# Performance work log

Measured on AMD Instinct MI355X. Metric: run time of the kernel, lower is better.

Reference implementation:

```python
import jax, jax.numpy as jnp
import numpy as np


def _lsa(cost):
    """Exact rectangular linear sum assignment (Jonker-Volgenant / e-maxx
    Hungarian with potentials). Returns (row_ind, col_ind) matching
    scipy.optimize.linear_sum_assignment (row_ind sorted ascending)."""
    n, m = cost.shape
    transposed = n > m
    if transposed:
        cost = cost.T
        n, m = m, n
    cost = np.asarray(cost, dtype=np.float64)
    INF = 1e18
    u = np.zeros(n + 1)
    v = np.zeros(m + 1)
    p = np.zeros(m + 1, dtype=np.int64)   # p[j]: 1-based row assigned to col j
    way = np.zeros(m + 1, dtype=np.int64)
    for i in range(1, n + 1):
        p[0] = i
        j0 = 0
        minv = np.full(m + 1, INF)
        used = np.zeros(m + 1, dtype=bool)
        while True:
            used[j0] = True
            i0 = p[j0]
            cur = cost[i0 - 1] - u[i0] - v[1:]          # vectorized over cols
            upd = (~used[1:]) & (cur < minv[1:])
            minv[1:] = np.where(upd, cur, minv[1:])
            way[1:] = np.where(upd, j0, way[1:])
            masked = np.where(used[1:], INF, minv[1:])
            j1 = int(np.argmin(masked)) + 1
            delta = masked[j1 - 1]
            u[p[used]] += delta
            v[used] -= delta
            minv[1:] = np.where(used[1:], minv[1:], minv[1:] - delta)
            j0 = j1
            if p[j0] == 0:
                break
        while j0 != 0:
            j1 = way[j0]
            p[j0] = p[j1]
            j0 = j1
    if transposed:
        pairs = sorted((j - 1, p[j] - 1) for j in range(1, m + 1) if p[j] != 0)
    else:
        pairs = sorted((p[j] - 1, j - 1) for j in range(1, m + 1) if p[j] != 0)
    row_ind = np.array([r for r, _ in pairs], dtype=np.int64)
    col_ind = np.array([c for _, c in pairs], dtype=np.int64)
    return row_ind, col_ind


def _row_order(cost_b):
    """Matched rows first (scipy order), then unmatched rows sorted ascending."""
    N = cost_b.shape[0]
    row_ind, _ = _lsa(cost_b)
    remain = sorted(set(range(N)) - set(row_ind.tolist()))
    return np.concatenate([row_ind, np.asarray(remain, dtype=np.int64)])


def _pairwise_l2(seq1, seq2):
    # Fused batched cdist: ||a-b|| = sqrt(|a|^2 + |b|^2 - 2 a.b)
    a2 = jnp.sum(seq1 * seq1, axis=-1)[:, :, None]   # [B,N,1]
    b2 = jnp.sum(seq2 * seq2, axis=-1)[:, None, :]   # [B,1,M]
    ab = jnp.einsum('bnd,bmd->bnm', seq1, seq2)      # [B,N,M]
    return jnp.sqrt(jnp.maximum(a2 + b2 - 2.0 * ab, 0.0))


def setup_inputs() -> dict:
    key = jax.random.key(0)
    k1, k2 = jax.random.split(key)
    B, N, M, D = 16, 512, 448, 1536
    return {
        'seq1': jax.random.normal(k1, (B, N, D), dtype=jnp.float32),
        'seq2': jax.random.normal(k2, (B, M, D), dtype=jnp.float32),
    }


def reference(seq1, seq2):
    cost = np.asarray(_pairwise_l2(seq1, seq2))      # [B,N,M], one fused kernel
    # Hungarian solve is inherently sequential / CPU-bound per batch element.
    perm = np.stack([_row_order(cost[b]) for b in range(cost.shape[0])], 0)
    perm = jnp.asarray(perm)                         # [B,N]
    return jnp.take_along_axis(seq1, perm[:, :, None], axis=1)
```

## Files before the change

kernel.cpp:

```cpp
#include <hip/hip_runtime.h>
#include <math.h>

#define BB 16
#define NN 512
#define MM 448
#define DD 1536

constexpr int TK = 32;

__global__ __launch_bounds__(256) void cost_kernel(const float* __restrict__ s1,
                                                   const float* __restrict__ s2,
                                                   float* __restrict__ Ct) {
  __shared__ float As[TK][68];
  __shared__ float Bs[TK][68];
  const int b = blockIdx.z;
  const int ibase = blockIdx.x * 64;
  const int jbase = blockIdx.y * 64;
  const int tid = threadIdx.x;
  const float* s1b = s1 + ((size_t)b * NN + ibase) * DD;
  const float* s2b = s2 + ((size_t)b * MM + jbase) * DD;
  const int ix = (tid & 15) * 4;
  const int jy = (tid >> 4) * 4;
  double acc[16];
#pragma unroll
  for (int t = 0; t < 16; ++t) acc[t] = 0.0;

  for (int k0 = 0; k0 < DD; k0 += TK) {
#pragma unroll
    for (int rep = 0; rep < 2; ++rep) {
      int idx = tid + rep * 256;
      int r = idx >> 3;
      int c4 = (idx & 7) * 4;
      float4 a = *(const float4*)(s1b + (size_t)r * DD + k0 + c4);
      As[c4 + 0][r] = a.x; As[c4 + 1][r] = a.y; As[c4 + 2][r] = a.z; As[c4 + 3][r] = a.w;
      float4 bb = *(const float4*)(s2b + (size_t)r * DD + k0 + c4);
      Bs[c4 + 0][r] = bb.x; Bs[c4 + 1][r] = bb.y; Bs[c4 + 2][r] = bb.z; Bs[c4 + 3][r] = bb.w;
    }
    __syncthreads();
    float pacc[16];
#pragma unroll
    for (int t = 0; t < 16; ++t) pacc[t] = 0.f;
#pragma unroll 8
    for (int kk = 0; kk < TK; ++kk) {
      float4 av = *(const float4*)&As[kk][ix];
      float4 bv = *(const float4*)&Bs[kk][jy];
      float a[4] = {av.x, av.y, av.z, av.w};
      float bq[4] = {bv.x, bv.y, bv.z, bv.w};
#pragma unroll
      for (int t = 0; t < 4; ++t)
#pragma unroll
        for (int q = 0; q < 4; ++q) {
          float d = a[t] - bq[q];
          pacc[t * 4 + q] = fmaf(d, d, pacc[t * 4 + q]);
        }
    }
#pragma unroll
    for (int t = 0; t < 16; ++t) acc[t] += (double)pacc[t];
    __syncthreads();
  }
#pragma unroll
  for (int t = 0; t < 4; ++t)
#pragma unroll
    for (int q = 0; q < 4; ++q) {
      int i = ibase + ix + t;
      int jj = jbase + jy + q;
      float d2 = (float)acc[t * 4 + q];
      Ct[((size_t)b * MM + jj) * NN + i] = sqrtf(fmaxf(d2, 0.f));
    }
}

__device__ __forceinline__ double wave_min_bcast_f64(double x) {
  union DU { double d; unsigned int u[2]; };
  DU v; v.d = x;
  DU inf; inf.d = 1e18;
#define DPP_STEP(CTRL) { DU o; \
  o.u[0] = (unsigned)__builtin_amdgcn_update_dpp((int)inf.u[0], (int)v.u[0], CTRL, 0xF, 0xF, false); \
  o.u[1] = (unsigned)__builtin_amdgcn_update_dpp((int)inf.u[1], (int)v.u[1], CTRL, 0xF, 0xF, false); \
  if (o.d < v.d) v.d = o.d; }
  DPP_STEP(0x111)
  DPP_STEP(0x112)
  DPP_STEP(0x114)
  DPP_STEP(0x118)
  DPP_STEP(0x142)
  DPP_STEP(0x143)
#undef DPP_STEP
  DU r;
  r.u[0] = (unsigned)__builtin_amdgcn_readlane((int)v.u[0], 63);
  r.u[1] = (unsigned)__builtin_amdgcn_readlane((int)v.u[1], 63);
  return r.d;
}

__global__ __launch_bounds__(64) void jv_kernel(const float* __restrict__ Ct,
                                                int* __restrict__ perm) {
  const int b = blockIdx.x;
  const float* C = Ct + (size_t)b * MM * NN;
  __shared__ double u_lds[MM + 1];
  __shared__ int p_lds[NN + 1];
  __shared__ int way_lds[NN + 1];
  __shared__ int cnt_lds[64];
  const int lane = threadIdx.x;
  const int jbase = 8 * lane + 1;

  for (int t = lane; t <= MM; t += 64) u_lds[t] = 0.0;
  for (int t = lane; t <= NN; t += 64) { p_lds[t] = 0; way_lds[t] = 0; }
  double vcol[8];
#pragma unroll
  for (int q = 0; q < 8; ++q) vcol[q] = 0.0;
  asm volatile("s_waitcnt lgkmcnt(0)" ::: "memory");

  for (int i = 1; i <= MM; ++i) {
    if (lane == 0) p_lds[0] = i;
    double minv[8], rec[8];
    int preg[8];
#pragma unroll
    for (int q = 0; q < 8; ++q) { minv[q] = 1e18; rec[q] = 0.0; preg[q] = 0; }
    int usedm = 0;
    double cum = 0.0;
    int j0 = 0, i0 = i;

    while (true) {
#pragma unroll
      for (int q = 0; q < 8; ++q)
        if (j0 == jbase + q) { usedm |= (1 << q); preg[q] = i0; rec[q] = cum; }

      const float4* r4 = (const float4*)(C + (size_t)(i0 - 1) * NN);
      float4 ca = r4[2 * lane];
      float4 cb = r4[2 * lane + 1];
      double uu = u_lds[i0];
      float c[8] = {ca.x, ca.y, ca.z, ca.w, cb.x, cb.y, cb.z, cb.w};
#pragma unroll
      for (int q = 0; q < 8; ++q) {
        if (!((usedm >> q) & 1)) {
          double cur = ((double)c[q] - uu) - vcol[q];
          if (cur < minv[q]) { minv[q] = cur; way_lds[jbase + q] = j0; }
        }
      }
      double cand = 1e18; int argj = 0;
#pragma unroll
      for (int q = 0; q < 8; ++q) {
        double mq = ((usedm >> q) & 1) ? 1e18 : minv[q];
        if (mq < cand) { cand = mq; argj = jbase + q; }
      }
      double delta = wave_min_bcast_f64(cand);
      unsigned long long bm = __ballot(cand == delta);
      int sl = (int)__ffsll((unsigned long long)bm) - 1;
      int j1 = __builtin_amdgcn_readlane(argj, sl);
      cum += delta;
#pragma unroll
      for (int q = 0; q < 8; ++q)
        if (!((usedm >> q) & 1)) minv[q] -= delta;
      int pn = p_lds[j1];
      j0 = j1;
      if (pn == 0) break;
      i0 = pn;
    }

    if (lane == 0) u_lds[i] += cum;
#pragma unroll
    for (int q = 0; q < 8; ++q)
      if ((usedm >> q) & 1) {
        double d = cum - rec[q];
        vcol[q] -= d;
        u_lds[preg[q]] += d;
      }
    asm volatile("s_waitcnt lgkmcnt(0)" ::: "memory");
    if (lane == 0) {
      int jj = j0;
      while (jj != 0) { int jp = way_lds[jj]; p_lds[jj] = p_lds[jp]; jj = jp; }
    }
    asm volatile("s_waitcnt lgkmcnt(0)" ::: "memory");
  }

  int mask = 0, cnt = 0;
#pragma unroll
  for (int q = 0; q < 8; ++q)
    if (p_lds[jbase + q] != 0) { mask |= 1 << q; cnt++; }
  cnt_lds[lane] = cnt;
  asm volatile("s_waitcnt lgkmcnt(0)" ::: "memory");
  int pre = 0;
  for (int l = 0; l < 64; ++l) { int cl = cnt_lds[l]; if (l < lane) pre += cl; }
  int mpos = pre;
  int upos = MM + (8 * lane - pre);
#pragma unroll
  for (int q = 0; q < 8; ++q) {
    int col = 8 * lane + q;
    if ((mask >> q) & 1) perm[b * NN + mpos++] = col;
    else                 perm[b * NN + upos++] = col;
  }
}

__global__ __launch_bounds__(256) void gather_kernel(const float* __restrict__ s1,
                                                     const int* __restrict__ perm,
                                                     float* __restrict__ out) {
  const int bi = blockIdx.x;
  const int b = bi >> 9;
  const int src = perm[bi];
  const float4* sp = (const float4*)(s1 + ((size_t)b * NN + src) * DD);
  float4* dp = (float4*)(out + (size_t)bi * DD);
  for (int t = threadIdx.x; t < DD / 4; t += 256) dp[t] = sp[t];
}

extern "C" void kernel_launch(void* const* d_in, const int* in_sizes, int n_in,
                              void* d_out, int out_size, void* d_ws, size_t ws_size,
                              hipStream_t stream) {
  const float* s1 = (const float*)d_in[0];
  const float* s2 = (const float*)d_in[1];
  float* out = (float*)d_out;
  float* Ct = (float*)d_out;
  int* perm = (int*)d_ws;

  dim3 cg(NN / 64, MM / 64, BB);
  cost_kernel<<<cg, 256, 0, stream>>>(s1, s2, Ct);
  jv_kernel<<<BB, 64, 0, stream>>>(Ct, perm);
  gather_kernel<<<BB * NN, 256, 0, stream>>>(s1, perm, out);
}
```

Measured before the change: 7.982 ms.

## Warm-start Hungarian solver with greedy row-minimum matching and dual potentials

Before the augmenting-path loop, each row's minimum cost and argmin column are computed with a wave reduction. The row potential is set to that minimum, and the row is greedily assigned to its argmin column when that column is free. Rows matched this way skip the sequential shortest-augmenting-path search, which cuts the dominant serial work. The risk is that when several optimal assignments exist, tie-breaking may differ from the reference, and the remaining augmentations may become longer.

```diff
diff --git a/kernel.cpp b/kernel.cpp
--- a/kernel.cpp
+++ b/kernel.cpp
@@ -90,6 +90,19 @@
   return r.d;
 }
 
+__device__ __forceinline__ float wave_min_bcast_f32(float x) {
+  union FU { float f; int i; };
+  FU v; v.f = x;
+  const int INFB = 0x7f7fffff;
+#define DPP1(CTRL) { FU o; \
+  o.i = __builtin_amdgcn_update_dpp(INFB, v.i, CTRL, 0xF, 0xF, false); \
+  if (o.f < v.f) v.f = o.f; }
+  DPP1(0x111) DPP1(0x112) DPP1(0x114) DPP1(0x118) DPP1(0x142) DPP1(0x143)
+#undef DPP1
+  FU r; r.i = __builtin_amdgcn_readlane(v.i, 63);
+  return r.f;
+}
+
 __global__ __launch_bounds__(64) void jv_kernel(const float* __restrict__ Ct,
                                                 int* __restrict__ perm) {
   const int b = blockIdx.x;
@@ -97,18 +110,47 @@
   __shared__ double u_lds[MM + 1];
   __shared__ int p_lds[NN + 1];
   __shared__ int way_lds[NN + 1];
+  __shared__ int colOwner[NN];
+  __shared__ int rowMatched[MM];
   __shared__ int cnt_lds[64];
   const int lane = threadIdx.x;
   const int jbase = 8 * lane + 1;
 
-  for (int t = lane; t <= MM; t += 64) u_lds[t] = 0.0;
+  if (lane == 0) u_lds[0] = 0.0;
   for (int t = lane; t <= NN; t += 64) { p_lds[t] = 0; way_lds[t] = 0; }
+  for (int t = lane; t < NN; t += 64) colOwner[t] = -1;
+  for (int t = lane; t < MM; t += 64) rowMatched[t] = 0;
+  asm volatile("s_waitcnt lgkmcnt(0)" ::: "memory");
+
+  for (int r = 0; r < MM; ++r) {
+    const float4* r4 = (const float4*)(C + (size_t)r * NN);
+    float4 ca = r4[2 * lane];
+    float4 cb = r4[2 * lane + 1];
+    float c[8] = {ca.x, ca.y, ca.z, ca.w, cb.x, cb.y, cb.z, cb.w};
+    float lm = 1e30f; int la = 0;
+#pragma unroll
+    for (int q = 0; q < 8; ++q)
+      if (c[q] < lm) { lm = c[q]; la = 8 * lane + q; }
+    float rm = wave_min_bcast_f32(lm);
+    unsigned long long bm = __ballot(lm == rm);
+    int sl = (int)__ffsll((unsigned long long)bm) - 1;
+    int jc = __builtin_amdgcn_readlane(la, sl);
+    if (lane == 0) {
+      u_lds[r + 1] = (double)rm;
+      if (colOwner[jc] < 0) {
+        colOwner[jc] = r;
+        rowMatched[r] = 1;
+        p_lds[jc + 1] = r + 1;
+      }
+    }
+  }
   double vcol[8];
 #pragma unroll
   for (int q = 0; q < 8; ++q) vcol[q] = 0.0;
   asm volatile("s_waitcnt lgkmcnt(0)" ::: "memory");
 
   for (int i = 1; i <= MM; ++i) {
+    if (rowMatched[i - 1]) continue;
     if (lane == 0) p_lds[0] = i;
     double minv[8], rec[8];
     int preg[8];
```

Result: no change. 7.996 ms (+0.2%).
